# Optimization experiments

Measured on AMD Instinct MI355X. Metric: run time of the kernel, lower is better.

## Reference

```python
import jax, jax.numpy as jnp
import numpy as np

D_MODEL = 1024
N_HEADS = 16
D_HEAD = D_MODEL // N_HEADS


def setup_inputs() -> dict:
    key = jax.random.key(0)
    ks = jax.random.split(key, 9)
    s = 1.0 / np.sqrt(D_MODEL)
    def lin(kw, kb):
        W = jax.random.uniform(kw, (D_MODEL, D_MODEL), jnp.float32, -s, s)
        b = jax.random.uniform(kb, (D_MODEL,), jnp.float32, -s, s)
        return W, b
    Wq, bq = lin(ks[0], ks[1])
    Wk, bk = lin(ks[2], ks[3])
    Wv, bv = lin(ks[4], ks[5])
    Wo, bo = lin(ks[6], ks[7])
    x = jax.random.normal(ks[8], (4, 2048, D_MODEL), jnp.float32)
    return {"x": x, "Wq": Wq, "bq": bq, "Wk": Wk, "bk": bk,
            "Wv": Wv, "bv": bv, "Wo": Wo, "bo": bo}


def reference(x, Wq, bq, Wk, bk, Wv, bv, Wo, bo):
    B, T, C = x.shape
    # torch Linear: y = x @ W.T + b
    Q = x @ Wq.T + bq
    K = x @ Wk.T + bk
    V = x @ Wv.T + bv
    # [B, H, T, Dh]
    Q = Q.reshape(B, T, N_HEADS, D_HEAD).transpose(0, 2, 1, 3)
    K = K.reshape(B, T, N_HEADS, D_HEAD).transpose(0, 2, 1, 3)
    V = V.reshape(B, T, N_HEADS, D_HEAD).transpose(0, 2, 1, 3)
    scale = jnp.float32(np.sqrt(D_HEAD))
    scores = jnp.einsum('bhqd,bhkd->bhqk', Q, K) / scale
    causal = jnp.tril(jnp.ones((T, T), dtype=bool))  # True where allowed
    scores = jnp.where(causal, scores, jnp.float32(-jnp.inf))
    attn = jax.nn.softmax(scores, axis=-1)
    out = jnp.einsum('bhqk,bhkd->bhqd', attn, V)
    out = out.transpose(0, 2, 1, 3).reshape(B, T, C)
    return out @ Wo.T + bo
```

## Files before the change

kernel.cpp:

```cpp
#include <hip/hip_runtime.h>
#include <hip/hip_bf16.h>


typedef float f32x4 __attribute__((ext_vector_type(4)));
typedef __bf16 bf16x8 __attribute__((ext_vector_type(8)));

#define DEVI __device__ __forceinline__

#define QSCALE 0.1803368801111204f

DEVI ushort f2b(float x) {
  __hip_bfloat16 h = __float2bfloat16(x);
  return __builtin_bit_cast(ushort, h);
}

DEVI ushort4 pack4(f32x4 v) {
  ushort4 o;
  o.x = f2b(v[0]); o.y = f2b(v[1]); o.z = f2b(v[2]); o.w = f2b(v[3]);
  return o;
}

DEVI bf16x8 ldsFrag(const ushort* p) {
  return __builtin_bit_cast(bf16x8, *(const uint4*)p);
}

DEVI f32x4 mfma16(bf16x8 a, bf16x8 b, f32x4 c) {
  return __builtin_amdgcn_mfma_f32_16x16x32_bf16(a, b, c, 0, 0, 0);
}

DEVI void gload_lds16(const ushort* g, ushort* l) {
  __builtin_amdgcn_global_load_lds(
      (const __attribute__((address_space(1))) unsigned int*)g,
      (__attribute__((address_space(3))) unsigned int*)l, 16, 0, 0);
}

__global__ void k_cvt(const float4* __restrict__ in, ushort4* __restrict__ out, int n4) {
  int i = blockIdx.x * 256 + threadIdx.x;
  if (i >= n4) return;
  float4 f = in[i];
  ushort4 o;
  o.x = f2b(f.x); o.y = f2b(f.y); o.z = f2b(f.z); o.w = f2b(f.w);
  out[i] = o;
}

__global__ void k_cvtW(const float4* __restrict__ w0, const float4* __restrict__ w1,
                       const float4* __restrict__ w2, const float4* __restrict__ w3,
                       ushort4* __restrict__ out) {
  const int y = blockIdx.y;
  const float4* src = (y == 0) ? w0 : (y == 1) ? w1 : (y == 2) ? w2 : w3;
  const int i = blockIdx.x * 256 + threadIdx.x;
  float4 f = src[i];
  ushort4 o;
  o.x = f2b(f.x); o.y = f2b(f.y); o.z = f2b(f.z); o.w = f2b(f.w);
  out[y * 262144 + i] = o;
}

template<int MODE>
__global__ __launch_bounds__(256)
void k_gemm(const ushort* __restrict__ A, const ushort* __restrict__ W,
            const float* __restrict__ b0, const float* __restrict__ b1,
            const float* __restrict__ b2, float* __restrict__ outF,
            ushort* __restrict__ oQ, ushort* __restrict__ oK, ushort* __restrict__ oV) {
  __shared__ ushort As[128 * 32];
  __shared__ ushort Bs[128 * 32];
  const int tid = threadIdx.x;
  const int wave = tid >> 6, lane = tid & 63;
  const int col = lane & 15, quad = lane >> 4;
  const int id = blockIdx.x;
  const int s_ = id >> 3;
  const int m0 = ((id & 7) * 8 + (s_ & 7)) * 128;
  const int n0 = (s_ >> 3) * 128;
  const int wm = (wave >> 1) * 64, wn = (wave & 1) * 64;
  f32x4 acc[4][4] = {};

  const int srow = wave * 16 + (lane >> 2);
  const int scol = (lane & 3) * 8;
  const ushort* Ag = A + (m0 + srow) * 1024 + scol;
  const ushort* Wg = W + (n0 + srow) * 1024 + scol;
  ushort* AsBase0 = &As[(wave * 16) * 32];
  ushort* AsBase1 = &As[(64 + wave * 16) * 32];
  ushort* BsBase0 = &Bs[(wave * 16) * 32];
  ushort* BsBase1 = &Bs[(64 + wave * 16) * 32];

  for (int k0 = 0; k0 < 1024; k0 += 32) {
    __syncthreads();
    gload_lds16(Ag + k0,             AsBase0);
    gload_lds16(Ag + 64 * 1024 + k0, AsBase1);
    gload_lds16(Wg + k0,             BsBase0);
    gload_lds16(Wg + 64 * 1024 + k0, BsBase1);
    __syncthreads();

    bf16x8 af[4], bfr[4];
#pragma unroll
    for (int i = 0; i < 4; ++i)
      af[i] = ldsFrag(&As[(wm + i * 16 + col) * 32 + quad * 8]);
#pragma unroll
    for (int j = 0; j < 4; ++j)
      bfr[j] = ldsFrag(&Bs[(wn + j * 16 + col) * 32 + quad * 8]);
#pragma unroll
    for (int i = 0; i < 4; ++i)
#pragma unroll
      for (int j = 0; j < 4; ++j)
        acc[i][j] = mfma16(af[i], bfr[j], acc[i][j]);
  }

  const int matId = (MODE == 0) ? (n0 >> 10) : 0;
  const float* bias = (MODE == 1) ? b0 : (matId == 0 ? b0 : (matId == 1 ? b1 : b2));
  const float sc = (MODE == 0 && matId == 0) ? QSCALE : 1.0f;
  ushort* outB = (MODE == 0) ? (matId == 0 ? oQ : (matId == 1 ? oK : oV)) : nullptr;

#pragma unroll
  for (int j = 0; j < 4; ++j) {
    const int n = n0 + wn + j * 16 + col;
    const int nl = n & 1023;
    const float bn = bias[nl];
#pragma unroll
    for (int i = 0; i < 4; ++i) {
      const int mBase = m0 + wm + i * 16 + quad * 4;
      if (MODE == 1) {
#pragma unroll
        for (int r = 0; r < 4; ++r)
          outF[(mBase + r) * 1024 + n] = acc[i][j][r] + bn;
      } else if (matId < 2) {
        const int h = nl >> 6, dh = nl & 63;
#pragma unroll
        for (int r = 0; r < 4; ++r) {
          const int m = mBase + r;
          const int b = m >> 11, t = m & 2047;
          outB[(((b * 16 + h) * 2048) + t) * 64 + dh] = f2b((acc[i][j][r] + bn) * sc);
        }
      } else {
        const int b = mBase >> 11, t = mBase & 2047;
        const int h = nl >> 6, dh = nl & 63;
        ushort4 pk;
        pk.x = f2b(acc[i][j][0] + bn);
        pk.y = f2b(acc[i][j][1] + bn);
        pk.z = f2b(acc[i][j][2] + bn);
        pk.w = f2b(acc[i][j][3] + bn);
        *(ushort4*)&outB[(((b * 16 + h) * 64) + dh) * 2048 + t] = pk;
      }
    }
  }
}

__global__ __launch_bounds__(256, 3)
void k_attn(const ushort* __restrict__ Q, const ushort* __restrict__ K,
            const ushort* __restrict__ Vt, ushort* __restrict__ AO) {
  __shared__ ushort Ks[2 * 64 * 32];
  __shared__ ushort Vs[2 * 80 * 32];
  __shared__ ushort Ps[4 * 2 * 16 * 72];
  const int tid = threadIdx.x;
  const int wave = tid >> 6, lane = tid & 63;
  const int col = lane & 15, quad = lane >> 4;
  const int id = blockIdx.x;
  const int sl = id >> 3;
  const int bh = (id & 7) * 8 + (sl & 7);
  const int t = sl >> 3;
  const int q0 = t * 128;
  const ushort* Qg = Q + (size_t)bh * 2048 * 64;
  const ushort* Kg = K + (size_t)bh * 2048 * 64;
  const ushort* Vg = Vt + (size_t)bh * 64 * 2048;

  {
    const int c = tid >> 7, w = tid & 127;
    const ushort one = 0x3F80;
    ushort4 zv;
    if (w < 8) { zv.x = one; zv.y = one; zv.z = one; zv.w = one; }
    else       { zv.x = 0;   zv.y = 0;   zv.z = 0;   zv.w = 0;   }
    *(ushort4*)&Vs[c * 2560 + 2048 + w * 4] = zv;
  }

  bf16x8 qf[2][2];
#pragma unroll
  for (int s = 0; s < 2; ++s) {
    const ushort* p = Qg + (q0 + wave * 32 + s * 16 + col) * 64 + quad * 8;
    qf[s][0] = __builtin_bit_cast(bf16x8, *(const uint4*)p);
    qf[s][1] = __builtin_bit_cast(bf16x8, *(const uint4*)(p + 32));
  }

  float mrow[2] = {-1e30f, -1e30f};
  f32x4 o[2][4] = {};
  f32x4 la[2] = {};

  const int srow = wave * 16 + (lane >> 2);
  const int scol = (lane & 3) * 8;
  const ushort* kPtr = Kg + srow * 64 + scol;
  const ushort* vPtr = Vg + srow * 2048 + scol;
  ushort* Ks0 = &Ks[(wave * 16) * 32];
  ushort* Ks1 = &Ks[(64 + wave * 16) * 32];
  ushort* Vs0 = &Vs[(wave * 16) * 32];
  ushort* Vs1 = &Vs[2560 + (wave * 16) * 32];
  ushort* Pw0 = &Ps[((wave * 2 + 0) * 16 + col) * 72];
  ushort* Pw1 = &Ps[((wave * 2 + 1) * 16 + col) * 72];

  auto stage = [&]() {
    gload_lds16(kPtr,      Ks0);
    gload_lds16(kPtr + 32, Ks1);
    gload_lds16(vPtr,      Vs0);
    gload_lds16(vPtr + 32, Vs1);
    kPtr += 64 * 64;
    vPtr += 64;
  };

  auto step = [&](bool masked, int d) {
    bf16x8 kf[4][2];
#pragma unroll
    for (int i = 0; i < 4; ++i) {
      kf[i][0] = ldsFrag(&Ks[(i * 16 + col) * 32 + quad * 8]);
      kf[i][1] = ldsFrag(&Ks[(64 + i * 16 + col) * 32 + quad * 8]);
    }
#pragma unroll
    for (int s = 0; s < 2; ++s) {
      const int exact = masked ? (2 * wave + s - 4 * d) : 99;
      f32x4 p[4];
      float tmax = -1e30f;
#pragma unroll
      for (int i = 0; i < 4; ++i) {
        if (i <= exact) {
          f32x4 z = {0.f, 0.f, 0.f, 0.f};
          f32x4 sv = mfma16(kf[i][0], qf[s][0], z);
          sv = mfma16(kf[i][1], qf[s][1], sv);
          if (masked && i == exact) {
#pragma unroll
            for (int r = 0; r < 4; ++r)
              if (quad * 4 + r > col) sv[r] = -1e30f;
          }
#pragma unroll
          for (int r = 0; r < 4; ++r) tmax = fmaxf(tmax, sv[r]);
          p[i] = sv;
        } else {
          p[i] = f32x4{0.f, 0.f, 0.f, 0.f};
        }
      }
      tmax = fmaxf(tmax, __shfl_xor(tmax, 16));
      tmax = fmaxf(tmax, __shfl_xor(tmax, 32));
      const float mnew = fmaxf(mrow[s], tmax);
      const float alpha = __builtin_amdgcn_exp2f(mrow[s] - mnew);
      mrow[s] = mnew;
#pragma unroll
      for (int i = 0; i < 4; ++i) {
        if (i <= exact) {
#pragma unroll
          for (int r = 0; r < 4; ++r)
            p[i][r] = __builtin_amdgcn_exp2f(p[i][r] - mnew);
        }
      }
      la[s] *= alpha;
#pragma unroll
      for (int i = 0; i < 4; ++i) o[s][i] *= alpha;
      ushort* Pw = s ? Pw1 : Pw0;
#pragma unroll
      for (int i = 0; i < 4; ++i)
        *(ushort4*)&Pw[i * 16 + quad * 4] = pack4(p[i]);
    }
#pragma unroll
    for (int c = 0; c < 2; ++c) {
      bf16x8 pb0 = ldsFrag(&Pw0[c * 32 + quad * 8]);
      bf16x8 pb1 = ldsFrag(&Pw1[c * 32 + quad * 8]);
      bf16x8 vone = ldsFrag(&Vs[(c * 80 + 64 + col) * 32 + quad * 8]);
      la[0] = mfma16(vone, pb0, la[0]);
      la[1] = mfma16(vone, pb1, la[1]);
#pragma unroll
      for (int i = 0; i < 4; ++i) {
        bf16x8 vf = ldsFrag(&Vs[(c * 80 + i * 16 + col) * 32 + quad * 8]);
        o[0][i] = mfma16(vf, pb0, o[0][i]);
        o[1][i] = mfma16(vf, pb1, o[1][i]);
      }
    }
  };

  const int nfull = 2 * t;
  for (int it = 0; it < nfull; ++it) {
    __syncthreads();
    stage();
    __syncthreads();
    step(false, 0);
  }
  __syncthreads();
  stage();
  __syncthreads();
  step(true, 0);
  __syncthreads();
  stage();
  __syncthreads();
  if (wave >= 2) step(true, 1);

  const int b = bh >> 4, h = bh & 15;
#pragma unroll
  for (int s = 0; s < 2; ++s) {
    const float l = __shfl(la[s][0], col);
    const float inv = 1.0f / l;
    const int tq = q0 + wave * 32 + s * 16 + col;
    ushort* dst = AO + (size_t)(b * 2048 + tq) * 1024 + h * 64;
#pragma unroll
    for (int i = 0; i < 4; ++i) {
      f32x4 v = o[s][i];
      v[0] *= inv; v[1] *= inv; v[2] *= inv; v[3] *= inv;
      *(ushort4*)&dst[i * 16 + quad * 4] = pack4(v);
    }
  }
}

extern "C" void kernel_launch(void* const* d_in, const int* in_sizes, int n_in,
                              void* d_out, int out_size, void* d_ws, size_t ws_size,
                              hipStream_t stream) {
  const float* x  = (const float*)d_in[0];
  const float* Wq = (const float*)d_in[1];
  const float* bq = (const float*)d_in[2];
  const float* Wk = (const float*)d_in[3];
  const float* bk = (const float*)d_in[4];
  const float* Wv = (const float*)d_in[5];
  const float* bv = (const float*)d_in[6];
  const float* Wo = (const float*)d_in[7];
  const float* bo = (const float*)d_in[8];
  float* out = (float*)d_out;

  char* ws = (char*)d_ws;
  ushort* xb    = (ushort*)ws;
  ushort* Wcat  = (ushort*)(ws + (size_t)16 * 1024 * 1024);
  ushort* Wob   = Wcat + (size_t)3 * 1024 * 1024;
  ushort* Qh    = (ushort*)(ws + (size_t)24 * 1024 * 1024);
  ushort* Kh    = Qh + (size_t)8192 * 1024;
  ushort* Vt    = Kh + (size_t)8192 * 1024;
  ushort* AO    = Vt + (size_t)8192 * 1024;

  k_cvt<<<8192, 256, 0, stream>>>((const float4*)x, (ushort4*)xb, 8192 * 1024 / 4);
  k_cvtW<<<dim3(1024, 4), 256, 0, stream>>>((const float4*)Wq, (const float4*)Wk,
                                            (const float4*)Wv, (const float4*)Wo,
                                            (ushort4*)Wcat);

  k_gemm<0><<<1536, 256, 0, stream>>>(xb, Wcat, bq, bk, bv, nullptr, Qh, Kh, Vt);

  k_attn<<<1024, 256, 0, stream>>>(Qh, Kh, Vt, AO);

  k_gemm<1><<<512, 256, 0, stream>>>(AO, Wob, bo, nullptr, nullptr, out,
                                     nullptr, nullptr, nullptr);
}
```

Baseline: 268.3 us.

## Pair causal query tiles per block and double-buffer K/V loads in attention

Each attention block now handles two query tiles, t and 15-t, so every block does the same amount of causal work. The grid is halved to 512. K/V staging moves to two LDS buffers, so the next tile's global-to-LDS load overlaps compute on the current one, with one barrier per iteration instead of two. Launch bounds drop from 3 to 2 blocks per CU to make room for the larger LDS footprint, which reduces occupancy.

```diff
diff --git a/kernel.cpp b/kernel.cpp
--- a/kernel.cpp
+++ b/kernel.cpp
@@ -143,20 +143,18 @@
   }
 }
 
-__global__ __launch_bounds__(256, 3)
+__global__ __launch_bounds__(256, 2)
 void k_attn(const ushort* __restrict__ Q, const ushort* __restrict__ K,
             const ushort* __restrict__ Vt, ushort* __restrict__ AO) {
-  __shared__ ushort Ks[2 * 64 * 32];
-  __shared__ ushort Vs[2 * 80 * 32];
+  __shared__ ushort Ks[2 * 4096];
+  __shared__ ushort Vs[2 * 5120];
   __shared__ ushort Ps[4 * 2 * 16 * 72];
   const int tid = threadIdx.x;
   const int wave = tid >> 6, lane = tid & 63;
   const int col = lane & 15, quad = lane >> 4;
   const int id = blockIdx.x;
-  const int sl = id >> 3;
-  const int bh = (id & 7) * 8 + (sl & 7);
-  const int t = sl >> 3;
-  const int q0 = t * 128;
+  const int bh = (id & 7) * 8 + ((id >> 3) & 7);
+  const int pr = id >> 6;
   const ushort* Qg = Q + (size_t)bh * 2048 * 64;
   const ushort* Kg = K + (size_t)bh * 2048 * 64;
   const ushort* Vg = Vt + (size_t)bh * 64 * 2048;
@@ -168,135 +166,138 @@
     if (w < 8) { zv.x = one; zv.y = one; zv.z = one; zv.w = one; }
     else       { zv.x = 0;   zv.y = 0;   zv.z = 0;   zv.w = 0;   }
     *(ushort4*)&Vs[c * 2560 + 2048 + w * 4] = zv;
+    *(ushort4*)&Vs[5120 + c * 2560 + 2048 + w * 4] = zv;
   }
-
-  bf16x8 qf[2][2];
-#pragma unroll
-  for (int s = 0; s < 2; ++s) {
-    const ushort* p = Qg + (q0 + wave * 32 + s * 16 + col) * 64 + quad * 8;
-    qf[s][0] = __builtin_bit_cast(bf16x8, *(const uint4*)p);
-    qf[s][1] = __builtin_bit_cast(bf16x8, *(const uint4*)(p + 32));
-  }
-
-  float mrow[2] = {-1e30f, -1e30f};
-  f32x4 o[2][4] = {};
-  f32x4 la[2] = {};
 
   const int srow = wave * 16 + (lane >> 2);
   const int scol = (lane & 3) * 8;
-  const ushort* kPtr = Kg + srow * 64 + scol;
-  const ushort* vPtr = Vg + srow * 2048 + scol;
-  ushort* Ks0 = &Ks[(wave * 16) * 32];
-  ushort* Ks1 = &Ks[(64 + wave * 16) * 32];
-  ushort* Vs0 = &Vs[(wave * 16) * 32];
-  ushort* Vs1 = &Vs[2560 + (wave * 16) * 32];
-  ushort* Pw0 = &Ps[((wave * 2 + 0) * 16 + col) * 72];
-  ushort* Pw1 = &Ps[((wave * 2 + 1) * 16 + col) * 72];
-
-  auto stage = [&]() {
-    gload_lds16(kPtr,      Ks0);
-    gload_lds16(kPtr + 32, Ks1);
-    gload_lds16(vPtr,      Vs0);
-    gload_lds16(vPtr + 32, Vs1);
-    kPtr += 64 * 64;
-    vPtr += 64;
-  };
-
-  auto step = [&](bool masked, int d) {
-    bf16x8 kf[4][2];
-#pragma unroll
-    for (int i = 0; i < 4; ++i) {
-      kf[i][0] = ldsFrag(&Ks[(i * 16 + col) * 32 + quad * 8]);
-      kf[i][1] = ldsFrag(&Ks[(64 + i * 16 + col) * 32 + quad * 8]);
+  const int ldsOff = srow * 32 + scol - (wave * 16) * 32;
+
+  for (int pp = 0; pp < 2; ++pp) {
+    const int t = pp ? (15 - pr) : pr;
+    const int q0 = t * 128;
+
+    bf16x8 qf[2][2];
+#pragma unroll
+    for (int s = 0; s < 2; ++s) {
+      const ushort* p = Qg + (q0 + wave * 32 + s * 16 + col) * 64 + quad * 8;
+      qf[s][0] = __builtin_bit_cast(bf16x8, *(const uint4*)p);
+      qf[s][1] = __builtin_bit_cast(bf16x8, *(const uint4*)(p + 32));
     }
+
+    float mrow[2] = {-1e30f, -1e30f};
+    f32x4 o[2][4] = {};
+    f32x4 la[2] = {};
+
+    const ushort* kPtr = Kg + srow * 64 + scol;
+    const ushort* vPtr = Vg + srow * 2048 + scol;
+    ushort* Pw0 = &Ps[((wave * 2 + 0) * 16 + col) * 72];
+    ushort* Pw1 = &Ps[((wave * 2 + 1) * 16 + col) * 72];
+
+    auto stage = [&](int buf) {
+      ushort* kb = &Ks[buf * 4096 + (wave * 16) * 32];
+      ushort* vb = &Vs[buf * 5120 + (wave * 16) * 32];
+      gload_lds16(kPtr,      kb);
+      gload_lds16(kPtr + 32, kb + 2048);
+      gload_lds16(vPtr,      vb);
+      gload_lds16(vPtr + 32, vb + 2560);
+      kPtr += 64 * 64;
+      vPtr += 64;
+    };
+
+    auto step = [&](int buf, bool masked, int d) {
+      const ushort* Kb = &Ks[buf * 4096];
+      const ushort* Vb = &Vs[buf * 5120];
+      bf16x8 kf[4][2];
+#pragma unroll
+      for (int i = 0; i < 4; ++i) {
+        kf[i][0] = ldsFrag(&Kb[(i * 16 + col) * 32 + quad * 8]);
+        kf[i][1] = ldsFrag(&Kb[(64 + i * 16 + col) * 32 + quad * 8]);
+      }
+#pragma unroll
+      for (int s = 0; s < 2; ++s) {
+        const int exact = masked ? (2 * wave + s - 4 * d) : 99;
+        f32x4 p[4];
+        float tmax = -1e30f;
+#pragma unroll
+        for (int i = 0; i < 4; ++i) {
+          if (i <= exact) {
+            f32x4 z = {0.f, 0.f, 0.f, 0.f};
+            f32x4 sv = mfma16(kf[i][0], qf[s][0], z);
+            sv = mfma16(kf[i][1], qf[s][1], sv);
+            if (masked && i == exact) {
+#pragma unroll
+              for (int r = 0; r < 4; ++r)
+                if (quad * 4 + r > col) sv[r] = -1e30f;
+            }
+#pragma unroll
+            for (int r = 0; r < 4; ++r) tmax = fmaxf(tmax, sv[r]);
+            p[i] = sv;
+          } else {
+            p[i] = f32x4{0.f, 0.f, 0.f, 0.f};
+          }
+        }
+        tmax = fmaxf(tmax, __shfl_xor(tmax, 16));
+        tmax = fmaxf(tmax, __shfl_xor(tmax, 32));
+        const float mnew = fmaxf(mrow[s], tmax);
+        const float alpha = __builtin_amdgcn_exp2f(mrow[s] - mnew);
+        mrow[s] = mnew;
+#pragma unroll
+        for (int i = 0; i < 4; ++i) {
+          if (i <= exact) {
+#pragma unroll
+            for (int r = 0; r < 4; ++r)
+              p[i][r] = __builtin_amdgcn_exp2f(p[i][r] - mnew);
+          }
+        }
+        la[s] *= alpha;
+#pragma unroll
+        for (int i = 0; i < 4; ++i) o[s][i] *= alpha;
+        ushort* Pw = s ? Pw1 : Pw0;
+#pragma unroll
+        for (int i = 0; i < 4; ++i)
+          *(ushort4*)&Pw[i * 16 + quad * 4] = pack4(p[i]);
+      }
+#pragma unroll
+      for (int c = 0; c < 2; ++c) {
+        bf16x8 pb0 = ldsFrag(&Pw0[c * 32 + quad * 8]);
+        bf16x8 pb1 = ldsFrag(&Pw1[c * 32 + quad * 8]);
+        bf16x8 vone = ldsFrag(&Vb[(c * 80 + 64 + col) * 32 + quad * 8]);
+        la[0] = mfma16(vone, pb0, la[0]);
+        la[1] = mfma16(vone, pb1, la[1]);
+#pragma unroll
+        for (int i = 0; i < 4; ++i) {
+          bf16x8 vf = ldsFrag(&Vb[(c * 80 + i * 16 + col) * 32 + quad * 8]);
+          o[0][i] = mfma16(vf, pb0, o[0][i]);
+          o[1][i] = mfma16(vf, pb1, o[1][i]);
+        }
+      }
+    };
+
+    const int ntiles = 2 * t + 2;
+    __syncthreads();
+    stage(0);
+    for (int it = 0; it < ntiles; ++it) {
+      __syncthreads();
+      if (it + 1 < ntiles) stage((it + 1) & 1);
+      if (it < 2 * t)           step(it & 1, false, 0);
+      else if (it == 2 * t)     step(it & 1, true, 0);
+      else if (wave >= 2)       step(it & 1, true, 1);
+    }
+
+    const float invs[2] = {1.0f / __shfl(la[0][0], col), 1.0f / __shfl(la[1][0], col)};
+    const int b = bh >> 4, h = bh & 15;
 #pragma unroll
     for (int s = 0; s < 2; ++s) {
-      const int exact = masked ? (2 * wave + s - 4 * d) : 99;
-      f32x4 p[4];
-      float tmax = -1e30f;
+      const float inv = invs[s];
+      const int tq = q0 + wave * 32 + s * 16 + col;
+      ushort* dst = AO + (size_t)(b * 2048 + tq) * 1024 + h * 64;
 #pragma unroll
       for (int i = 0; i < 4; ++i) {
-        if (i <= exact) {
-          f32x4 z = {0.f, 0.f, 0.f, 0.f};
-          f32x4 sv = mfma16(kf[i][0], qf[s][0], z);
-          sv = mfma16(kf[i][1], qf[s][1], sv);
-          if (masked && i == exact) {
-#pragma unroll
-            for (int r = 0; r < 4; ++r)
-              if (quad * 4 + r > col) sv[r] = -1e30f;
-          }
-#pragma unroll
-          for (int r = 0; r < 4; ++r) tmax = fmaxf(tmax, sv[r]);
-          p[i] = sv;
-        } else {
-          p[i] = f32x4{0.f, 0.f, 0.f, 0.f};
-        }
-      }
-      tmax = fmaxf(tmax, __shfl_xor(tmax, 16));
-      tmax = fmaxf(tmax, __shfl_xor(tmax, 32));
-      const float mnew = fmaxf(mrow[s], tmax);
-      const float alpha = __builtin_amdgcn_exp2f(mrow[s] - mnew);
-      mrow[s] = mnew;
-#pragma unroll
-      for (int i = 0; i < 4; ++i) {
-        if (i <= exact) {
-#pragma unroll
-          for (int r = 0; r < 4; ++r)
-            p[i][r] = __builtin_amdgcn_exp2f(p[i][r] - mnew);
-        }
-      }
-      la[s] *= alpha;
-#pragma unroll
-      for (int i = 0; i < 4; ++i) o[s][i] *= alpha;
-      ushort* Pw = s ? Pw1 : Pw0;
-#pragma unroll
-      for (int i = 0; i < 4; ++i)
-        *(ushort4*)&Pw[i * 16 + quad * 4] = pack4(p[i]);
-    }
-#pragma unroll
-    for (int c = 0; c < 2; ++c) {
-      bf16x8 pb0 = ldsFrag(&Pw0[c * 32 + quad * 8]);
-      bf16x8 pb1 = ldsFrag(&Pw1[c * 32 + quad * 8]);
-      bf16x8 vone = ldsFrag(&Vs[(c * 80 + 64 + col) * 32 + quad * 8]);
-      la[0] = mfma16(vone, pb0, la[0]);
-      la[1] = mfma16(vone, pb1, la[1]);
-#pragma unroll
-      for (int i = 0; i < 4; ++i) {
-        bf16x8 vf = ldsFrag(&Vs[(c * 80 + i * 16 + col) * 32 + quad * 8]);
-        o[0][i] = mfma16(vf, pb0, o[0][i]);
-        o[1][i] = mfma16(vf, pb1, o[1][i]);
-      }
-    }
-  };
-
-  const int nfull = 2 * t;
-  for (int it = 0; it < nfull; ++it) {
-    __syncthreads();
-    stage();
-    __syncthreads();
-    step(false, 0);
-  }
-  __syncthreads();
-  stage();
-  __syncthreads();
-  step(true, 0);
-  __syncthreads();
-  stage();
-  __syncthreads();
-  if (wave >= 2) step(true, 1);
-
-  const int b = bh >> 4, h = bh & 15;
-#pragma unroll
-  for (int s = 0; s < 2; ++s) {
-    const float l = __shfl(la[s][0], col);
-    const float inv = 1.0f / l;
-    const int tq = q0 + wave * 32 + s * 16 + col;
-    ushort* dst = AO + (size_t)(b * 2048 + tq) * 1024 + h * 64;
-#pragma unroll
-    for (int i = 0; i < 4; ++i) {
-      f32x4 v = o[s][i];
-      v[0] *= inv; v[1] *= inv; v[2] *= inv; v[3] *= inv;
-      *(ushort4*)&dst[i * 16 + quad * 4] = pack4(v);
+        f32x4 v = o[s][i];
+        v[0] *= inv; v[1] *= inv; v[2] *= inv; v[3] *= inv;
+        *(ushort4*)&dst[i * 16 + quad * 4] = pack4(v);
+      }
     }
   }
 }
@@ -331,7 +332,7 @@
 
   k_gemm<0><<<1536, 256, 0, stream>>>(xb, Wcat, bq, bk, bv, nullptr, Qh, Kh, Vt);
 
-  k_attn<<<1024, 256, 0, stream>>>(Qh, Kh, Vt, AO);
+  k_attn<<<512, 256, 0, stream>>>(Qh, Kh, Vt, AO);
 
   k_gemm<1><<<512, 256, 0, stream>>>(AO, Wob, bo, nullptr, nullptr, out,
                                      nullptr, nullptr, nullptr);
```

Result: no change. 264.3 us (-1.5%).
